# Performance work log

Hardware: AMD Instinct MI355X
Metric: run time of the kernel (lower is better)

Reference implementation:

```python
import jax, jax.numpy as jnp
import numpy as np

B, N, D, H, FF, L = 4, 256, 240, 8, 1024, 4
HD = D // H  # 30, divisible by 3 for 3D rotary
EPS = 1e-5


def setup_inputs() -> dict:
    key = jax.random.key(0)
    ks = iter(jax.random.split(key, 40))
    def nrm(shape, scale=1.0):
        return jax.random.normal(next(ks), shape, jnp.float32) * scale
    inp = {}
    for n in ["hand_token_t", "head_token_t", "hand_token_m1", "head_token_m1"]:
        inp[n] = nrm((B, N, D))
    for n in ["coords_hand_t", "coords_head_t", "coords_hand_m1", "coords_head_m1"]:
        inp[n] = jax.random.uniform(next(ks), (B, N, 3), jnp.float32)
    for n in ["state_t", "state_m1", "hand_pose_m1", "head_pose_m1", "hand_pose_t", "head_pose_t"]:
        inp[n] = nrm((B, D))
    sd = float(np.sqrt(2.0 / D))   # kaiming_normal fan_in=D
    sf = float(np.sqrt(2.0 / FF))  # kaiming_normal fan_in=FF
    inp["Wq"] = nrm((L, D, D), sd); inp["Wk"] = nrm((L, D, D), sd)
    inp["Wv"] = nrm((L, D, D), sd); inp["Wo"] = nrm((L, D, D), sd)
    inp["W1"] = nrm((L, FF, D), sd); inp["W2"] = nrm((L, D, FF), sf)
    inp["bq"] = jnp.zeros((L, D)); inp["bk"] = jnp.zeros((L, D))
    inp["bv"] = jnp.zeros((L, D)); inp["bo"] = jnp.zeros((L, D))
    inp["b1"] = jnp.zeros((L, FF)); inp["b2"] = jnp.zeros((L, D))
    inp["g1"] = jnp.ones((L, D)); inp["be1"] = jnp.zeros((L, D))
    inp["g2"] = jnp.ones((L, D)); inp["be2"] = jnp.zeros((L, D))
    return inp


def rope3d(x, coords):
    # x: (B,H,S,HD); coords: (B,S,3). head_dim split into 3 axis blocks,
    # each block rotated (interleaved pairs) by RoPE with pos = coord along that axis.
    d = HD // 3
    inv = 1.0 / (10000.0 ** (jnp.arange(0, d, 2, dtype=jnp.float32) / d))  # (d//2,)
    outs = []
    for a in range(3):
        xa = x[..., a * d:(a + 1) * d]
        ang = coords[:, None, :, a, None] * inv  # (B,1,S,d//2)
        c, s = jnp.cos(ang), jnp.sin(ang)
        x1, x2 = xa[..., 0::2], xa[..., 1::2]
        outs.append(jnp.stack([x1 * c - x2 * s, x1 * s + x2 * c], -1).reshape(xa.shape))
    if HD % 3:
        outs.append(x[..., 3 * d:])
    return jnp.concatenate(outs, -1)


def layernorm(x, g, b):
    m = x.mean(-1, keepdims=True)
    v = jnp.mean((x - m) ** 2, -1, keepdims=True)
    return (x - m) * jax.lax.rsqrt(v + EPS) * g + b


def _forward(hand_token_t, head_token_t, hand_token_m1, head_token_m1,
             coords_hand_t, coords_head_t, coords_hand_m1, coords_head_m1,
             state_t, state_m1, hand_pose_m1, head_pose_m1, hand_pose_t, head_pose_t,
             Wq, bq, Wk, bk, Wv, bv, Wo, bo, W1, b1, W2, b2, g1, be1, g2, be2):
    z3 = jnp.zeros((B, 1, 3), jnp.float32)
    src = jnp.concatenate([
        state_m1[:, None], hand_pose_m1[:, None], head_pose_m1[:, None],
        hand_token_m1, head_token_m1,
        state_t[:, None], hand_pose_t[:, None], head_pose_t[:, None],
        hand_token_t, head_token_t], axis=1)            # (B, S, D)
    cs = jnp.concatenate([z3, z3, z3, coords_hand_m1, coords_head_m1,
                          z3, z3, z3, coords_hand_t, coords_head_t], axis=1)  # (B, S, 3)
    S = src.shape[1]
    past = 1 + 2 + 2 * N  # current-frame tokens hide the past-frame keys
    mask = jnp.zeros((S, S), bool).at[past:, :past].set(True)
    scale = 1.0 / float(np.sqrt(HD))
    for l in range(L):
        q = (src @ Wq[l].T + bq[l]).reshape(B, S, H, HD).transpose(0, 2, 1, 3)
        k = (src @ Wk[l].T + bk[l]).reshape(B, S, H, HD).transpose(0, 2, 1, 3)
        v = (src @ Wv[l].T + bv[l]).reshape(B, S, H, HD).transpose(0, 2, 1, 3)
        q = rope3d(q, cs)
        k = rope3d(k, cs)
        scores = jnp.einsum('bhqd,bhkd->bhqk', q, k) * scale
        scores = jnp.where(mask, -jnp.inf, scores)
        attn = jnp.einsum('bhqk,bhkd->bhqd', jax.nn.softmax(scores, axis=-1), v)
        attn = attn.transpose(0, 2, 1, 3).reshape(B, S, D)
        s2 = layernorm(src + attn @ Wo[l].T + bo[l], g1[l], be1[l])
        ff = jax.nn.gelu(s2 @ W1[l].T + b1[l], approximate=False) @ W2[l].T + b2[l]
        src = layernorm(s2 + ff, g2[l], be2[l])
    return src[:, past:, :]


def reference(hand_token_t, head_token_t, hand_token_m1, head_token_m1,
              coords_hand_t, coords_head_t, coords_hand_m1, coords_head_m1,
              state_t, state_m1, hand_pose_m1, head_pose_m1, hand_pose_t, head_pose_t,
              Wq, bq, Wk, bk, Wv, bv, Wo, bo, W1, b1, W2, b2, g1, be1, g2, be2):
    return _forward(hand_token_t, head_token_t, hand_token_m1, head_token_m1,
                    coords_hand_t, coords_head_t, coords_hand_m1, coords_head_m1,
                    state_t, state_m1, hand_pose_m1, head_pose_m1, hand_pose_t, head_pose_t,
                    Wq, bq, Wk, bk, Wv, bv, Wo, bo, W1, b1, W2, b2, g1, be1, g2, be2)
```

## Files before the change

### kernel.cpp

```cpp
#include <hip/hip_runtime.h>
#include <cmath>

constexpr int cB = 4, cN = 256, cD = 240, cH = 8, cFF = 1024, cL = 4;
constexpr int cHD = 30;
constexpr int cS2 = 515;
constexpr int cBS2 = cB * cS2;
constexpr int cKp = 256;
constexpr int cSP2 = 576;
constexpr float EPSF = 1e-5f;

typedef __bf16 bf16x8 __attribute__((ext_vector_type(8)));
typedef float f32x4 __attribute__((ext_vector_type(4)));

__device__ inline unsigned short f2bf(float f) {
    unsigned int u = __builtin_bit_cast(unsigned int, f);
    unsigned int r = (u + 0x7fffu + ((u >> 16) & 1u)) >> 16;
    return (unsigned short)r;
}

constexpr int R1 = 4 * cL * 65536;
constexpr int R2 = R1 + cL * 1024 * 256;
constexpr int R3 = R2 + cL * 256 * 1024;
constexpr int R4 = R3 + cBS2 * cD;
constexpr int R5 = R4 + cBS2 * 15;
constexpr size_t qkvN = (size_t)cB * cH * cSP2 * 32;
constexpr int nSpan32 = (int)(3 * qkvN / 2);
constexpr int R6 = R5 + nSpan32;
constexpr int R7 = R6 + cBS2 * 8;

__global__ __launch_bounds__(256) void setup_all(
    const float* __restrict__ Wq, const float* __restrict__ Wk,
    const float* __restrict__ Wv, const float* __restrict__ Wo,
    const float* __restrict__ W1, const float* __restrict__ W2,
    const float* __restrict__ hand_t, const float* __restrict__ head_t,
    const float* __restrict__ state_t,
    const float* __restrict__ hand_pose_t, const float* __restrict__ head_pose_t,
    const float* __restrict__ ch_t, const float* __restrict__ cd_t,
    unsigned short* __restrict__ wqkv, unsigned short* __restrict__ w1p,
    unsigned short* __restrict__ w2p,
    float* __restrict__ src, unsigned short* __restrict__ sbf,
    float2* __restrict__ trig,
    unsigned int* __restrict__ qkvspan,
    unsigned short* __restrict__ padA, unsigned short* __restrict__ padB,
    unsigned short* __restrict__ padC)
{
    int idx = blockIdx.x * 256 + threadIdx.x;
    if (idx < R1) {
        int which = idx >> 18;
        const float* W = (which == 0) ? Wq : (which == 1) ? Wk : (which == 2) ? Wv : Wo;
        int rem = idx & 262143;
        int m = rem >> 16;
        int rc = rem & 65535;
        int r = rc >> 8, c = rc & 255;
        float v = (r < 240 && c < 240) ? W[((size_t)m * 240 + r) * 240 + c] : 0.f;
        wqkv[idx] = f2bf(v);
    } else if (idx < R2) {
        int rem = idx - R1;
        int m = rem >> 18;
        int rc = rem & 262143;
        int r = rc >> 8, c = rc & 255;
        float v = (c < 240) ? W1[((size_t)m * 1024 + r) * 240 + c] : 0.f;
        w1p[rem] = f2bf(v);
    } else if (idx < R3) {
        int rem = idx - R2;
        int m = rem >> 18;
        int rc = rem & 262143;
        int r = rc >> 10, c = rc & 1023;
        float v = (r < 240) ? W2[((size_t)m * 240 + r) * 1024 + c] : 0.f;
        w2p[rem] = f2bf(v);
    } else if (idx < R4) {
        int rem = idx - R3;
        int d = rem % cD;
        int r = rem / cD;
        int b = r / cS2, s = r % cS2;
        const float* p; int off;
        if (s == 0)          { p = state_t;      off = b * cD + d; }
        else if (s == 1)     { p = hand_pose_t;  off = b * cD + d; }
        else if (s == 2)     { p = head_pose_t;  off = b * cD + d; }
        else if (s < 259)    { p = hand_t;       off = (b * cN + (s - 3)) * cD + d; }
        else                 { p = head_t;       off = (b * cN + (s - 259)) * cD + d; }
        float v = p[off];
        src[rem] = v;
        sbf[(size_t)r * cKp + d] = f2bf(v);
    } else if (idx < R5) {
        int rem = idx - R4;
        int r = rem / 15, pair = rem - r * 15;
        int b = r / cS2, s = r % cS2;
        int a = pair / 5, j = pair - a * 5;
        float coord = 0.f;
        if (s >= 3 && s < 259)       coord = ch_t[(b * cN + (s - 3)) * 3 + a];
        else if (s >= 259)           coord = cd_t[(b * cN + (s - 259)) * 3 + a];
        float inv = __expf(-1.8420680743952367f * (float)j);
        float sn, co;
        sincosf(coord * inv, &sn, &co);
        trig[rem] = make_float2(co, sn);
    } else if (idx < R6) {
        qkvspan[idx - R5] = 0u;
    } else if (idx < R7) {
        int rem = idx - R6;
        int r = rem >> 3, j = rem & 7;
        ((unsigned int*)(padA + (size_t)r * 256 + 240))[j] = 0u;
        ((unsigned int*)(padB + (size_t)r * 256 + 240))[j] = 0u;
        ((unsigned int*)(padC + (size_t)r * 256 + 240))[j] = 0u;
    }
}

#define GEMM_CORE64(A_PTR, W_PTR, M_, KA_, NK_)                                               \
    __shared__ unsigned short Al[64][72];                                                     \
    __shared__ unsigned short Bl[64][72];                                                     \
    const int tid = threadIdx.x;                                                              \
    const int lane = tid & 63;                                                                \
    const int w = tid >> 6;                                                                   \
    const int wm = w >> 1, wn = w & 1;                                                        \
    const int lrow = lane & 15, kq = lane >> 4;                                               \
    const int colBase = blockIdx.x * 64;                                                      \
    const int sRow = tid >> 2;                                                                \
    const int sC = (tid & 3) * 16;                                                            \
    const int ar0 = min(rowBase + sRow, M_ - 1);                                              \
    const int wr = colBase + sRow;                                                            \
    const unsigned short* a0p = A_PTR + (size_t)ar0 * KA_ + sC;                               \
    const unsigned short* wp  = W_PTR + (size_t)wr * KA_ + sC;                                \
    f32x4 acc[2][2] = {};                                                                     \
    int4 rA0a = *(const int4*)a0p, rA0b = *(const int4*)(a0p + 8);                            \
    int4 rBa  = *(const int4*)wp,  rBb  = *(const int4*)(wp + 8);                             \
    for (int ks = 0; ks < NK_; ++ks) {                                                        \
        __syncthreads();                                                                      \
        *(int4*)&Al[sRow][sC]     = rA0a;                                                     \
        *(int4*)&Al[sRow][sC + 8] = rA0b;                                                     \
        *(int4*)&Bl[sRow][sC]     = rBa;                                                      \
        *(int4*)&Bl[sRow][sC + 8] = rBb;                                                      \
        __syncthreads();                                                                      \
        if (ks + 1 < NK_) {                                                                   \
            int kk = (ks + 1) * 64;                                                           \
            rA0a = *(const int4*)(a0p + kk); rA0b = *(const int4*)(a0p + kk + 8);             \
            rBa  = *(const int4*)(wp + kk);  rBb  = *(const int4*)(wp + kk + 8);              \
        }                                                                                     \
        _Pragma("unroll")                                                                     \
        for (int sub = 0; sub < 2; ++sub) {                                                   \
            bf16x8 af[2], bfr[2];                                                             \
            _Pragma("unroll")                                                                 \
            for (int i = 0; i < 2; ++i)                                                       \
                af[i] = *(const bf16x8*)&Al[wm * 32 + i * 16 + lrow][sub * 32 + kq * 8];      \
            _Pragma("unroll")                                                                 \
            for (int j = 0; j < 2; ++j)                                                       \
                bfr[j] = *(const bf16x8*)&Bl[wn * 32 + j * 16 + lrow][sub * 32 + kq * 8];     \
            _Pragma("unroll")                                                                 \
            for (int i = 0; i < 2; ++i)                                                       \
                _Pragma("unroll")                                                             \
                for (int j = 0; j < 2; ++j)                                                   \
                    acc[i][j] = __builtin_amdgcn_mfma_f32_16x16x32_bf16(af[i], bfr[j], acc[i][j], 0, 0, 0); \
        }                                                                                     \
    }

__global__ __launch_bounds__(256) void gemm_qkv_rope(
    const unsigned short* __restrict__ A,
    const unsigned short* __restrict__ Wqp, const unsigned short* __restrict__ Wkp,
    const unsigned short* __restrict__ Wvp,
    const float* __restrict__ bq, const float* __restrict__ bk, const float* __restrict__ bv,
    const float2* __restrict__ trig,
    unsigned short* __restrict__ qbf, unsigned short* __restrict__ kbf,
    unsigned short* __restrict__ vtbf)
{
    const int z = blockIdx.z;
    const unsigned short* Wsel = (z == 0) ? Wqp : (z == 1) ? Wkp : Wvp;
    const float* bias = (z == 0) ? bq : (z == 1) ? bk : bv;
    const int rowBase = blockIdx.y * 64;
    GEMM_CORE64(A, Wsel, cBS2, cKp, 4)
    if (z == 2) {
#pragma unroll
        for (int i = 0; i < 2; ++i) {
#pragma unroll
            for (int j = 0; j < 2; ++j) {
                int col = colBase + wn * 32 + j * 16 + lrow;
                if (col >= cD) continue;
                float bcol = bias[col];
                int hh = col / cHD, hd = col % cHD;
                f32x4 vv = acc[i][j];
                int row0 = rowBase + wm * 32 + i * 16 + kq * 4;
                int b0 = row0 / cS2, s0 = row0 - b0 * cS2;
                if (row0 + 3 < cBS2 && s0 + 3 < cS2) {
                    unsigned int lo = (unsigned)f2bf(vv[0] + bcol) | ((unsigned)f2bf(vv[1] + bcol) << 16);
                    unsigned int hi = (unsigned)f2bf(vv[2] + bcol) | ((unsigned)f2bf(vv[3] + bcol) << 16);
                    size_t base = ((size_t)(b0 * cH + hh) * 32 + hd) * cSP2 + s0;
                    *(unsigned int*)&vtbf[base]     = lo;
                    *(unsigned int*)&vtbf[base + 2] = hi;
                } else {
#pragma unroll
                    for (int r = 0; r < 4; ++r) {
                        int row = row0 + r;
                        if (row >= cBS2) continue;
                        int bb = row / cS2, ss = row - bb * cS2;
                        vtbf[((size_t)(bb * cH + hh) * 32 + hd) * cSP2 + ss] = f2bf(vv[r] + bcol);
                    }
                }
            }
        }
    } else {
        unsigned short* dst = (z == 0) ? qbf : kbf;
#pragma unroll
        for (int i = 0; i < 2; ++i) {
#pragma unroll
            for (int j = 0; j < 2; ++j) {
                int col = colBase + wn * 32 + j * 16 + lrow;
                bool colok = col < cD;
                int cc = colok ? col : 0;
                float bcol = colok ? bias[cc] : 0.f;
                int hh = cc / cHD, hd = cc % cHD;
                int a3 = hd / 10, jj = (hd % 10) >> 1;
                int pair = a3 * 5 + jj;
                f32x4 vv = acc[i][j];
#pragma unroll
                for (int r = 0; r < 4; ++r) {
                    int row = rowBase + wm * 32 + i * 16 + kq * 4 + r;
                    bool rowok = row < cBS2;
                    int rowc = rowok ? row : 0;
                    float val = vv[r] + bcol;
                    float pval = __shfl_xor(val, 1);
                    float2 t = trig[rowc * 15 + pair];
                    float outv = (hd & 1) ? (pval * t.y + val * t.x) : (val * t.x - pval * t.y);
                    if (colok && rowok) {
                        int b = rowc / cS2, s = rowc - b * cS2;
                        dst[((size_t)(b * cH + hh) * cSP2 + s) * 32 + hd] = f2bf(outv);
                    }
                }
            }
        }
    }
}

__global__ __launch_bounds__(256) void attn_mfma(
    const unsigned short* __restrict__ qbf, const unsigned short* __restrict__ kbf,
    const unsigned short* __restrict__ vtbf, unsigned short* __restrict__ outb)
{
    __shared__ unsigned short Pl[4][16][72];
    __shared__ float Ol[4][16][33];
    __shared__ float Ml[4][16];
    __shared__ float Ll[4][16];
    const int tid = threadIdx.x, lane = tid & 63, w = tid >> 6;
    const int bh = blockIdx.y, b = bh >> 3, h = bh & 7;
    const int qbase = blockIdx.x * 16;
    const int lr = lane & 15, lg = lane >> 4;
    const float scl = 0.18257418583505536f;
    const f32x4 czero = {0.f, 0.f, 0.f, 0.f};
    bf16x8 qf = *(const bf16x8*)&qbf[((size_t)bh * cSP2 + qbase + lr) * 32 + lg * 8];
    float m[4], l[4];
    f32x4 o0 = czero, o1 = czero;
#pragma unroll
    for (int r = 0; r < 4; ++r) { m[r] = -3.0e38f; l[r] = 0.f; }
    const int ts = (w * 9) / 4;
    const int te = ((w + 1) * 9) / 4;
    for (int tt = ts; tt < te; ++tt) {
        const int kb = tt * 64;
        f32x4 c[4];
#pragma unroll
        for (int t = 0; t < 4; ++t) {
            bf16x8 kf = *(const bf16x8*)&kbf[((size_t)bh * cSP2 + kb + 16 * t + lr) * 32 + lg * 8];
            c[t] = __builtin_amdgcn_mfma_f32_16x16x32_bf16(qf, kf, czero, 0, 0, 0);
        }
#pragma unroll
        for (int t = 0; t < 4; ++t) {
            bool koob = (kb + 16 * t + lr) >= cS2;
#pragma unroll
            for (int r = 0; r < 4; ++r)
                c[t][r] = koob ? -3.0e38f : c[t][r] * scl;
        }
        float mx[4];
#pragma unroll
        for (int r = 0; r < 4; ++r)
            mx[r] = fmaxf(fmaxf(c[0][r], c[1][r]), fmaxf(c[2][r], c[3][r]));
#pragma unroll
        for (int off = 1; off < 16; off <<= 1)
#pragma unroll
            for (int r = 0; r < 4; ++r)
                mx[r] = fmaxf(mx[r], __shfl_xor(mx[r], off));
        float corr[4], me[4], ps[4];
#pragma unroll
        for (int r = 0; r < 4; ++r) {
            float mn = fmaxf(m[r], mx[r]);
            corr[r] = __expf(m[r] - mn);
            m[r] = mn;
            me[r] = fmaxf(mn, -1.0e30f);
            ps[r] = 0.f;
        }
#pragma unroll
        for (int t = 0; t < 4; ++t)
#pragma unroll
            for (int r = 0; r < 4; ++r) {
                float p = __expf(c[t][r] - me[r]);
                c[t][r] = p;
                ps[r] += p;
            }
#pragma unroll
        for (int off = 1; off < 16; off <<= 1)
#pragma unroll
            for (int r = 0; r < 4; ++r)
                ps[r] += __shfl_xor(ps[r], off);
#pragma unroll
        for (int r = 0; r < 4; ++r) {
            l[r] = l[r] * corr[r] + ps[r];
            o0[r] *= corr[r];
            o1[r] *= corr[r];
        }
#pragma unroll
        for (int t = 0; t < 4; ++t)
#pragma unroll
            for (int r = 0; r < 4; ++r)
                Pl[w][lg * 4 + r][16 * t + lr] = f2bf(c[t][r]);
#pragma unroll
        for (int c2 = 0; c2 < 2; ++c2) {
            bf16x8 pa  = *(const bf16x8*)&Pl[w][lr][c2 * 32 + lg * 8];
            bf16x8 bv0 = *(const bf16x8*)&vtbf[((size_t)bh * 32 + lr) * cSP2 + kb + c2 * 32 + lg * 8];
            bf16x8 bv1 = *(const bf16x8*)&vtbf[((size_t)bh * 32 + 16 + lr) * cSP2 + kb + c2 * 32 + lg * 8];
            o0 = __builtin_amdgcn_mfma_f32_16x16x32_bf16(pa, bv0, o0, 0, 0, 0);
            o1 = __builtin_amdgcn_mfma_f32_16x16x32_bf16(pa, bv1, o1, 0, 0, 0);
        }
    }
#pragma unroll
    for (int r = 0; r < 4; ++r) {
        int row = lg * 4 + r;
        if (lr == 0) { Ml[w][row] = m[r]; Ll[w][row] = l[r]; }
        Ol[w][row][lr]      = o0[r];
        Ol[w][row][16 + lr] = o1[r];
    }
    __syncthreads();
    if (w == 0) {
        const int col = lane & 31, half = lane >> 5;
#pragma unroll
        for (int rr = 0; rr < 8; ++rr) {
            int row = half * 8 + rr;
            float M = fmaxf(fmaxf(Ml[0][row], Ml[1][row]), fmaxf(Ml[2][row], Ml[3][row]));
            float Lt = 0.f, Ot = 0.f;
#pragma unroll
            for (int ww = 0; ww < 4; ++ww) {
                float cc = __expf(Ml[ww][row] - M);
                Lt += Ll[ww][row] * cc;
                Ot += Ol[ww][row][col] * cc;
            }
            int qq = qbase + row;
            if (qq < cS2 && col < cHD)
                outb[((size_t)(b * cS2 + qq)) * cKp + h * cHD + col] = f2bf(Ot / Lt);
        }
    }
}

__global__ __launch_bounds__(256) void gemm_res64(
    const unsigned short* __restrict__ A, const unsigned short* __restrict__ W,
    const float* __restrict__ bias, const float* __restrict__ Rs,
    float* __restrict__ outF)
{
    const int rowBase = blockIdx.y * 64;
    GEMM_CORE64(A, W, cBS2, cKp, 4)
#pragma unroll
    for (int i = 0; i < 2; ++i) {
#pragma unroll
        for (int j = 0; j < 2; ++j) {
            int col = colBase + wn * 32 + j * 16 + lrow;
            if (col >= cD) continue;
            float bcol = bias[col];
            f32x4 v = acc[i][j];
#pragma unroll
            for (int r = 0; r < 4; ++r) {
                int row = rowBase + wm * 32 + i * 16 + kq * 4 + r;
                if (row >= cBS2) continue;
                outF[(size_t)row * cD + col] = v[r] + bcol + Rs[(size_t)row * cD + col];
            }
        }
    }
}

__global__ __launch_bounds__(256) void gemm_ff1(
    const unsigned short* __restrict__ A, const unsigned short* __restrict__ W,
    const float* __restrict__ bias, unsigned short* __restrict__ outB)
{
    const int rowBase = blockIdx.y * 64;
    GEMM_CORE64(A, W, cBS2, cKp, 4)
#pragma unroll
    for (int i = 0; i < 2; ++i) {
#pragma unroll
        for (int j = 0; j < 2; ++j) {
            int col = colBase + wn * 32 + j * 16 + lrow;
            float bcol = bias[col];
            f32x4 v = acc[i][j];
#pragma unroll
            for (int r = 0; r < 4; ++r) {
                int row = rowBase + wm * 32 + i * 16 + kq * 4 + r;
                if (row >= cBS2) continue;
                float t = v[r] + bcol;
                float gl = 0.5f * t * (1.0f + erff(t * 0.70710678118654752f));
                outB[(size_t)row * 1024 + col] = f2bf(gl);
            }
        }
    }
}

__global__ __launch_bounds__(256) void gemm_ff2_part(
    const unsigned short* __restrict__ A, const unsigned short* __restrict__ W,
    float* __restrict__ p0, float* __restrict__ p1)
{
    const int z = blockIdx.z;
    const int rowBase = blockIdx.y * 64;
    const unsigned short* Ap = A + z * 512;
    const unsigned short* Wp = W + z * 512;
    float* pF = z ? p1 : p0;
    GEMM_CORE64(Ap, Wp, cBS2, cFF, 8)
#pragma unroll
    for (int i = 0; i < 2; ++i) {
#pragma unroll
        for (int j = 0; j < 2; ++j) {
            int col = colBase + wn * 32 + j * 16 + lrow;
            if (col >= cD) continue;
            f32x4 v = acc[i][j];
#pragma unroll
            for (int r = 0; r < 4; ++r) {
                int row = rowBase + wm * 32 + i * 16 + kq * 4 + r;
                if (row >= cBS2) continue;
                pF[(size_t)row * cD + col] = v[r];
            }
        }
    }
}

__device__ inline void ln_core(float4 v, const float* __restrict__ g,
                               const float* __restrict__ be, float* __restrict__ yr,
                               unsigned short* __restrict__ br, int lane, bool ok)
{
    float sum = v.x + v.y + v.z + v.w;
#pragma unroll
    for (int off = 1; off < 64; off <<= 1) sum += __shfl_xor(sum, off);
    float mean = sum * (1.0f / cD);
    float vs = 0.f;
    if (ok) {
        float dx = v.x - mean, dy = v.y - mean, dz = v.z - mean, dw = v.w - mean;
        vs = dx * dx + dy * dy + dz * dz + dw * dw;
    }
#pragma unroll
    for (int off = 1; off < 64; off <<= 1) vs += __shfl_xor(vs, off);
    float rstd = rsqrtf(vs * (1.0f / cD) + EPSF);
    if (ok) {
        float4 g4 = *(const float4*)(g + 4 * lane);
        float4 b4 = *(const float4*)(be + 4 * lane);
        float4 y;
        y.x = (v.x - mean) * rstd * g4.x + b4.x;
        y.y = (v.y - mean) * rstd * g4.y + b4.y;
        y.z = (v.z - mean) * rstd * g4.z + b4.z;
        y.w = (v.w - mean) * rstd * g4.w + b4.w;
        *(float4*)(yr + 4 * lane) = y;
        if (br) {
            uint2 pk;
            pk.x = (unsigned)f2bf(y.x) | ((unsigned)f2bf(y.y) << 16);
            pk.y = (unsigned)f2bf(y.z) | ((unsigned)f2bf(y.w) << 16);
            *(uint2*)(br + 4 * lane) = pk;
        }
    }
}

__global__ __launch_bounds__(256) void ln_kernel(
    const float* __restrict__ x, const float* __restrict__ g,
    const float* __restrict__ be, float* __restrict__ y, unsigned short* __restrict__ ybf)
{
    int row = blockIdx.x * 4 + (threadIdx.x >> 6);
    int lane = threadIdx.x & 63;
    if (row >= cBS2) return;
    bool ok = lane < 60;
    float4 v = make_float4(0.f, 0.f, 0.f, 0.f);
    if (ok) v = *(const float4*)(x + (size_t)row * cD + 4 * lane);
    ln_core(v, g, be, y + (size_t)row * cD, ybf + (size_t)row * cKp, lane, ok);
}

__global__ __launch_bounds__(256) void ln2_kernel(
    const float* __restrict__ s2, const float* __restrict__ p0, const float* __restrict__ p1,
    const float* __restrict__ b2, const float* __restrict__ g, const float* __restrict__ be,
    float* __restrict__ y, unsigned short* __restrict__ ybf)
{
    int row = blockIdx.x * 4 + (threadIdx.x >> 6);
    int lane = threadIdx.x & 63;
    if (row >= cBS2) return;
    bool ok = lane < 60;
    float4 v = make_float4(0.f, 0.f, 0.f, 0.f);
    if (ok) {
        float4 a  = *(const float4*)(s2 + (size_t)row * cD + 4 * lane);
        float4 q0 = *(const float4*)(p0 + (size_t)row * cD + 4 * lane);
        float4 q1 = *(const float4*)(p1 + (size_t)row * cD + 4 * lane);
        float4 bb = *(const float4*)(b2 + 4 * lane);
        v.x = a.x + q0.x + q1.x + bb.x;
        v.y = a.y + q0.y + q1.y + bb.y;
        v.z = a.z + q0.z + q1.z + bb.z;
        v.w = a.w + q0.w + q1.w + bb.w;
    }
    ln_core(v, g, be, y + (size_t)row * cD, ybf + (size_t)row * cKp, lane, ok);
}

__global__ __launch_bounds__(256) void ln2_final(
    const float* __restrict__ s2, const float* __restrict__ p0, const float* __restrict__ p1,
    const float* __restrict__ b2, const float* __restrict__ g, const float* __restrict__ be,
    float* __restrict__ out)
{
    int row = blockIdx.x * 4 + (threadIdx.x >> 6);
    int lane = threadIdx.x & 63;
    if (row >= cBS2) return;
    bool ok = lane < 60;
    float4 v = make_float4(0.f, 0.f, 0.f, 0.f);
    if (ok) {
        float4 a  = *(const float4*)(s2 + (size_t)row * cD + 4 * lane);
        float4 q0 = *(const float4*)(p0 + (size_t)row * cD + 4 * lane);
        float4 q1 = *(const float4*)(p1 + (size_t)row * cD + 4 * lane);
        float4 bb = *(const float4*)(b2 + 4 * lane);
        v.x = a.x + q0.x + q1.x + bb.x;
        v.y = a.y + q0.y + q1.y + bb.y;
        v.z = a.z + q0.z + q1.z + bb.z;
        v.w = a.w + q0.w + q1.w + bb.w;
    }
    ln_core(v, g, be, out + (size_t)row * cD, nullptr, lane, ok);
}

extern "C" void kernel_launch(void* const* d_in, const int* in_sizes, int n_in,
                              void* d_out, int out_size, void* d_ws, size_t ws_size,
                              hipStream_t stream) {
    (void)in_sizes; (void)n_in; (void)out_size; (void)ws_size;
    const float* hand_t       = (const float*)d_in[0];
    const float* head_t       = (const float*)d_in[1];
    const float* c_hand_t     = (const float*)d_in[4];
    const float* c_head_t     = (const float*)d_in[5];
    const float* state_t      = (const float*)d_in[8];
    const float* hand_pose_t  = (const float*)d_in[12];
    const float* head_pose_t  = (const float*)d_in[13];
    const float* Wq = (const float*)d_in[14];
    const float* Wk = (const float*)d_in[15];
    const float* Wv = (const float*)d_in[16];
    const float* Wo = (const float*)d_in[17];
    const float* W1 = (const float*)d_in[18];
    const float* W2 = (const float*)d_in[19];
    const float* bq = (const float*)d_in[20];
    const float* bk = (const float*)d_in[21];
    const float* bv = (const float*)d_in[22];
    const float* bo = (const float*)d_in[23];
    const float* b1 = (const float*)d_in[24];
    const float* b2 = (const float*)d_in[25];
    const float* g1 = (const float*)d_in[26];
    const float* be1 = (const float*)d_in[27];
    const float* g2 = (const float*)d_in[28];
    const float* be2 = (const float*)d_in[29];

    char* p = (char*)d_ws;
    auto alloc_f = [&](size_t n) { float* r = (float*)p; p += n * sizeof(float); return r; };
    auto alloc_h = [&](size_t n) { unsigned short* r = (unsigned short*)p; p += n * sizeof(unsigned short); return r; };
    float* srcb  = alloc_f((size_t)cBS2 * cD);
    float* s2b   = alloc_f((size_t)cBS2 * cD);
    float* resid = alloc_f((size_t)cBS2 * cD);
    float* part1 = alloc_f((size_t)cBS2 * cD);
    float* trigf = alloc_f((size_t)cBS2 * 15 * 2);
    unsigned short* src_bf  = alloc_h((size_t)cBS2 * cKp);
    unsigned short* s2_bf   = alloc_h((size_t)cBS2 * cKp);
    unsigned short* attn_bf = alloc_h((size_t)cBS2 * cKp);
    unsigned short* ff_bf   = alloc_h((size_t)cBS2 * cFF);
    unsigned short* qbf  = alloc_h(qkvN);
    unsigned short* kbf  = alloc_h(qkvN);
    unsigned short* vtbf = alloc_h(qkvN);
    unsigned short* wqkv = alloc_h((size_t)4 * cL * 65536);
    unsigned short* w1p  = alloc_h((size_t)cL * 1024 * 256);
    unsigned short* w2p  = alloc_h((size_t)cL * 256 * 1024);
    float2* trig = (float2*)trigf;

    setup_all<<<(R7 + 255) / 256, 256, 0, stream>>>(
        Wq, Wk, Wv, Wo, W1, W2,
        hand_t, head_t, state_t, hand_pose_t, head_pose_t,
        c_hand_t, c_head_t,
        wqkv, w1p, w2p, srcb, src_bf, trig,
        (unsigned int*)qbf, src_bf, s2_bf, attn_bf);

    const int mT = (cBS2 + 63) / 64;
    for (int l = 0; l < cL; ++l) {
        const unsigned short* wq_l = wqkv + (size_t)(0 * cL + l) * 65536;
        const unsigned short* wk_l = wqkv + (size_t)(1 * cL + l) * 65536;
        const unsigned short* wv_l = wqkv + (size_t)(2 * cL + l) * 65536;
        const unsigned short* wo_l = wqkv + (size_t)(3 * cL + l) * 65536;
        const unsigned short* w1_l = w1p + (size_t)l * 1024 * 256;
        const unsigned short* w2_l = w2p + (size_t)l * 256 * 1024;
        const float* bq_l = bq + (size_t)l * cD;
        const float* bk_l = bk + (size_t)l * cD;
        const float* bv_l = bv + (size_t)l * cD;
        const float* bo_l = bo + (size_t)l * cD;
        const float* b1_l = b1 + (size_t)l * cFF;
        const float* b2_l = b2 + (size_t)l * cD;
        const float* g1_l = g1 + (size_t)l * cD;
        const float* be1_l = be1 + (size_t)l * cD;
        const float* g2_l = g2 + (size_t)l * cD;
        const float* be2_l = be2 + (size_t)l * cD;

        gemm_qkv_rope<<<dim3(4, mT, 3), 256, 0, stream>>>(
            src_bf, wq_l, wk_l, wv_l, bq_l, bk_l, bv_l, trig, qbf, kbf, vtbf);
        attn_mfma<<<dim3((cS2 + 15) / 16, cB * cH), 256, 0, stream>>>(
            qbf, kbf, vtbf, attn_bf);
        gemm_res64<<<dim3(4, mT), 256, 0, stream>>>(
            attn_bf, wo_l, bo_l, srcb, resid);
        ln_kernel<<<(cBS2 + 3) / 4, 256, 0, stream>>>(resid, g1_l, be1_l, s2b, s2_bf);
        gemm_ff1<<<dim3(16, mT), 256, 0, stream>>>(s2_bf, w1_l, b1_l, ff_bf);
        gemm_ff2_part<<<dim3(4, mT, 2), 256, 0, stream>>>(ff_bf, w2_l, resid, part1);
        if (l < cL - 1) {
            ln2_kernel<<<(cBS2 + 3) / 4, 256, 0, stream>>>(
                s2b, resid, part1, b2_l, g2_l, be2_l, srcb, src_bf);
        } else {
            ln2_final<<<(cBS2 + 3) / 4, 256, 0, stream>>>(
                s2b, resid, part1, b2_l, g2_l, be2_l, (float*)d_out);
        }
    }
}
```

Baseline: 247.5 us.

## Fuse layernorms into preceding GEMMs via last-block atomic counter

Removes the standalone ln_kernel, ln2_kernel and ln2_final launches. Each row-tile's last-finishing GEMM block, found with an atomic counter per row tile and thread fences, now does the layernorm for those 64 rows. This saves kernel launches and an extra pass over the activations each layer. In exchange, only one block per row tile does the LN work serially at the end, and correctness relies on fences and on resetting the counters.

```diff
diff --git a/kernel.cpp b/kernel.cpp
--- a/kernel.cpp
+++ b/kernel.cpp
@@ -27,6 +27,7 @@
 constexpr int nSpan32 = (int)(3 * qkvN / 2);
 constexpr int R6 = R5 + nSpan32;
 constexpr int R7 = R6 + cBS2 * 8;
+constexpr int R8 = R7 + 128;
 
 __global__ __launch_bounds__(256) void setup_all(
     const float* __restrict__ Wq, const float* __restrict__ Wk,
@@ -42,7 +43,8 @@
     float2* __restrict__ trig,
     unsigned int* __restrict__ qkvspan,
     unsigned short* __restrict__ padA, unsigned short* __restrict__ padB,
-    unsigned short* __restrict__ padC)
+    unsigned short* __restrict__ padC,
+    unsigned int* __restrict__ cnts)
 {
     int idx = blockIdx.x * 256 + threadIdx.x;
     if (idx < R1) {
@@ -102,6 +104,8 @@
         ((unsigned int*)(padA + (size_t)r * 256 + 240))[j] = 0u;
         ((unsigned int*)(padB + (size_t)r * 256 + 240))[j] = 0u;
         ((unsigned int*)(padC + (size_t)r * 256 + 240))[j] = 0u;
+    } else if (idx < R8) {
+        cnts[idx - R7] = 0u;
     }
 }
 
@@ -128,7 +132,7 @@
         *(int4*)&Al[sRow][sC]     = rA0a;                                                     \
         *(int4*)&Al[sRow][sC + 8] = rA0b;                                                     \
         *(int4*)&Bl[sRow][sC]     = rBa;                                                      \
-        *(int4*)&Bl[sRow][sC + 8] = rBb;                                                      \
+        *(int4*)&Bl[sRow][sC + 8] = rBb;                                                     \
         __syncthreads();                                                                      \
         if (ks + 1 < NK_) {                                                                   \
             int kk = (ks + 1) * 64;                                                           \
@@ -152,6 +156,40 @@
         }                                                                                     \
     }
 
+__device__ inline void ln_core(float4 v, const float* __restrict__ g,
+                               const float* __restrict__ be, float* __restrict__ yr,
+                               unsigned short* __restrict__ br, int lane, bool ok)
+{
+    float sum = v.x + v.y + v.z + v.w;
+#pragma unroll
+    for (int off = 1; off < 64; off <<= 1) sum += __shfl_xor(sum, off);
+    float mean = sum * (1.0f / cD);
+    float vs = 0.f;
+    if (ok) {
+        float dx = v.x - mean, dy = v.y - mean, dz = v.z - mean, dw = v.w - mean;
+        vs = dx * dx + dy * dy + dz * dz + dw * dw;
+    }
+#pragma unroll
+    for (int off = 1; off < 64; off <<= 1) vs += __shfl_xor(vs, off);
+    float rstd = rsqrtf(vs * (1.0f / cD) + EPSF);
+    if (ok) {
+        float4 g4 = *(const float4*)(g + 4 * lane);
+        float4 b4 = *(const float4*)(be + 4 * lane);
+        float4 y;
+        y.x = (v.x - mean) * rstd * g4.x + b4.x;
+        y.y = (v.y - mean) * rstd * g4.y + b4.y;
+        y.z = (v.z - mean) * rstd * g4.z + b4.z;
+        y.w = (v.w - mean) * rstd * g4.w + b4.w;
+        *(float4*)(yr + 4 * lane) = y;
+        if (br) {
+            uint2 pk;
+            pk.x = (unsigned)f2bf(y.x) | ((unsigned)f2bf(y.y) << 16);
+            pk.y = (unsigned)f2bf(y.z) | ((unsigned)f2bf(y.w) << 16);
+            *(uint2*)(br + 4 * lane) = pk;
+        }
+    }
+}
+
 __global__ __launch_bounds__(256) void gemm_qkv_rope(
     const unsigned short* __restrict__ A,
     const unsigned short* __restrict__ Wqp, const unsigned short* __restrict__ Wkp,
@@ -343,10 +381,13 @@
     }
 }
 
-__global__ __launch_bounds__(256) void gemm_res64(
+__global__ __launch_bounds__(256) void gemm_res64_ln(
     const unsigned short* __restrict__ A, const unsigned short* __restrict__ W,
     const float* __restrict__ bias, const float* __restrict__ Rs,
-    float* __restrict__ outF)
+    float* __restrict__ outF,
+    const float* __restrict__ g, const float* __restrict__ be,
+    float* __restrict__ yF, unsigned short* __restrict__ yB,
+    unsigned int* __restrict__ cnt)
 {
     const int rowBase = blockIdx.y * 64;
     GEMM_CORE64(A, W, cBS2, cKp, 4)
@@ -364,6 +405,26 @@
                 if (row >= cBS2) continue;
                 outF[(size_t)row * cD + col] = v[r] + bcol + Rs[(size_t)row * cD + col];
             }
+        }
+    }
+    __threadfence();
+    __syncthreads();
+    __shared__ int lastBlk;
+    if (tid == 0) {
+        unsigned int old = atomicAdd(&cnt[blockIdx.y], 1u);
+        lastBlk = (old == 3u);
+        if (old == 3u) cnt[blockIdx.y] = 0u;
+    }
+    __syncthreads();
+    if (lastBlk) {
+        __threadfence();
+        for (int rr = w; rr < 64; rr += 4) {
+            int row = rowBase + rr;
+            if (row >= cBS2) break;
+            bool ok = lane < 60;
+            float4 v = make_float4(0.f, 0.f, 0.f, 0.f);
+            if (ok) v = *(const float4*)(outF + (size_t)row * cD + 4 * lane);
+            ln_core(v, g, be, yF + (size_t)row * cD, yB + (size_t)row * cKp, lane, ok);
         }
     }
 }
@@ -393,9 +454,14 @@
     }
 }
 
-__global__ __launch_bounds__(256) void gemm_ff2_part(
+template<int FIN>
+__global__ __launch_bounds__(256) void gemm_ff2_ln(
     const unsigned short* __restrict__ A, const unsigned short* __restrict__ W,
-    float* __restrict__ p0, float* __restrict__ p1)
+    float* __restrict__ p0, float* __restrict__ p1,
+    const float* __restrict__ s2, const float* __restrict__ b2,
+    const float* __restrict__ g, const float* __restrict__ be,
+    float* __restrict__ yF, unsigned short* __restrict__ yB,
+    unsigned int* __restrict__ cnt)
 {
     const int z = blockIdx.z;
     const int rowBase = blockIdx.y * 64;
@@ -418,99 +484,36 @@
             }
         }
     }
-}
-
-__device__ inline void ln_core(float4 v, const float* __restrict__ g,
-                               const float* __restrict__ be, float* __restrict__ yr,
-                               unsigned short* __restrict__ br, int lane, bool ok)
-{
-    float sum = v.x + v.y + v.z + v.w;
-#pragma unroll
-    for (int off = 1; off < 64; off <<= 1) sum += __shfl_xor(sum, off);
-    float mean = sum * (1.0f / cD);
-    float vs = 0.f;
-    if (ok) {
-        float dx = v.x - mean, dy = v.y - mean, dz = v.z - mean, dw = v.w - mean;
-        vs = dx * dx + dy * dy + dz * dz + dw * dw;
-    }
-#pragma unroll
-    for (int off = 1; off < 64; off <<= 1) vs += __shfl_xor(vs, off);
-    float rstd = rsqrtf(vs * (1.0f / cD) + EPSF);
-    if (ok) {
-        float4 g4 = *(const float4*)(g + 4 * lane);
-        float4 b4 = *(const float4*)(be + 4 * lane);
-        float4 y;
-        y.x = (v.x - mean) * rstd * g4.x + b4.x;
-        y.y = (v.y - mean) * rstd * g4.y + b4.y;
-        y.z = (v.z - mean) * rstd * g4.z + b4.z;
-        y.w = (v.w - mean) * rstd * g4.w + b4.w;
-        *(float4*)(yr + 4 * lane) = y;
-        if (br) {
-            uint2 pk;
-            pk.x = (unsigned)f2bf(y.x) | ((unsigned)f2bf(y.y) << 16);
-            pk.y = (unsigned)f2bf(y.z) | ((unsigned)f2bf(y.w) << 16);
-            *(uint2*)(br + 4 * lane) = pk;
-        }
-    }
-}
-
-__global__ __launch_bounds__(256) void ln_kernel(
-    const float* __restrict__ x, const float* __restrict__ g,
-    const float* __restrict__ be, float* __restrict__ y, unsigned short* __restrict__ ybf)
-{
-    int row = blockIdx.x * 4 + (threadIdx.x >> 6);
-    int lane = threadIdx.x & 63;
-    if (row >= cBS2) return;
-    bool ok = lane < 60;
-    float4 v = make_float4(0.f, 0.f, 0.f, 0.f);
-    if (ok) v = *(const float4*)(x + (size_t)row * cD + 4 * lane);
-    ln_core(v, g, be, y + (size_t)row * cD, ybf + (size_t)row * cKp, lane, ok);
-}
-
-__global__ __launch_bounds__(256) void ln2_kernel(
-    const float* __restrict__ s2, const float* __restrict__ p0, const float* __restrict__ p1,
-    const float* __restrict__ b2, const float* __restrict__ g, const float* __restrict__ be,
-    float* __restrict__ y, unsigned short* __restrict__ ybf)
-{
-    int row = blockIdx.x * 4 + (threadIdx.x >> 6);
-    int lane = threadIdx.x & 63;
-    if (row >= cBS2) return;
-    bool ok = lane < 60;
-    float4 v = make_float4(0.f, 0.f, 0.f, 0.f);
-    if (ok) {
-        float4 a  = *(const float4*)(s2 + (size_t)row * cD + 4 * lane);
-        float4 q0 = *(const float4*)(p0 + (size_t)row * cD + 4 * lane);
-        float4 q1 = *(const float4*)(p1 + (size_t)row * cD + 4 * lane);
-        float4 bb = *(const float4*)(b2 + 4 * lane);
-        v.x = a.x + q0.x + q1.x + bb.x;
-        v.y = a.y + q0.y + q1.y + bb.y;
-        v.z = a.z + q0.z + q1.z + bb.z;
-        v.w = a.w + q0.w + q1.w + bb.w;
-    }
-    ln_core(v, g, be, y + (size_t)row * cD, ybf + (size_t)row * cKp, lane, ok);
-}
-
-__global__ __launch_bounds__(256) void ln2_final(
-    const float* __restrict__ s2, const float* __restrict__ p0, const float* __restrict__ p1,
-    const float* __restrict__ b2, const float* __restrict__ g, const float* __restrict__ be,
-    float* __restrict__ out)
-{
-    int row = blockIdx.x * 4 + (threadIdx.x >> 6);
-    int lane = threadIdx.x & 63;
-    if (row >= cBS2) return;
-    bool ok = lane < 60;
-    float4 v = make_float4(0.f, 0.f, 0.f, 0.f);
-    if (ok) {
-        float4 a  = *(const float4*)(s2 + (size_t)row * cD + 4 * lane);
-        float4 q0 = *(const float4*)(p0 + (size_t)row * cD + 4 * lane);
-        float4 q1 = *(const float4*)(p1 + (size_t)row * cD + 4 * lane);
-        float4 bb = *(const float4*)(b2 + 4 * lane);
-        v.x = a.x + q0.x + q1.x + bb.x;
-        v.y = a.y + q0.y + q1.y + bb.y;
-        v.z = a.z + q0.z + q1.z + bb.z;
-        v.w = a.w + q0.w + q1.w + bb.w;
-    }
-    ln_core(v, g, be, out + (size_t)row * cD, nullptr, lane, ok);
+    __threadfence();
+    __syncthreads();
+    __shared__ int lastBlk;
+    if (tid == 0) {
+        unsigned int old = atomicAdd(&cnt[blockIdx.y], 1u);
+        lastBlk = (old == 7u);
+        if (old == 7u) cnt[blockIdx.y] = 0u;
+    }
+    __syncthreads();
+    if (lastBlk) {
+        __threadfence();
+        for (int rr = w; rr < 64; rr += 4) {
+            int row = rowBase + rr;
+            if (row >= cBS2) break;
+            bool ok = lane < 60;
+            float4 v = make_float4(0.f, 0.f, 0.f, 0.f);
+            if (ok) {
+                float4 a  = *(const float4*)(s2 + (size_t)row * cD + 4 * lane);
+                float4 q0 = *(const float4*)(p0 + (size_t)row * cD + 4 * lane);
+                float4 q1 = *(const float4*)(p1 + (size_t)row * cD + 4 * lane);
+                float4 bb = *(const float4*)(b2 + 4 * lane);
+                v.x = a.x + q0.x + q1.x + bb.x;
+                v.y = a.y + q0.y + q1.y + bb.y;
+                v.z = a.z + q0.z + q1.z + bb.z;
+                v.w = a.w + q0.w + q1.w + bb.w;
+            }
+            ln_core(v, g, be, yF + (size_t)row * cD,
+                    FIN ? nullptr : (yB + (size_t)row * cKp), lane, ok);
+        }
+    }
 }
 
 extern "C" void kernel_launch(void* const* d_in, const int* in_sizes, int n_in,
@@ -549,6 +552,7 @@
     float* resid = alloc_f((size_t)cBS2 * cD);
     float* part1 = alloc_f((size_t)cBS2 * cD);
     float* trigf = alloc_f((size_t)cBS2 * 15 * 2);
+    unsigned int* cnts = (unsigned int*)alloc_f(128);
     unsigned short* src_bf  = alloc_h((size_t)cBS2 * cKp);
     unsigned short* s2_bf   = alloc_h((size_t)cBS2 * cKp);
     unsigned short* attn_bf = alloc_h((size_t)cBS2 * cKp);
@@ -560,13 +564,15 @@
     unsigned short* w1p  = alloc_h((size_t)cL * 1024 * 256);
     unsigned short* w2p  = alloc_h((size_t)cL * 256 * 1024);
     float2* trig = (float2*)trigf;
-
-    setup_all<<<(R7 + 255) / 256, 256, 0, stream>>>(
+    unsigned int* cntA = cnts;
+    unsigned int* cntB = cnts + 64;
+
+    setup_all<<<(R8 + 255) / 256, 256, 0, stream>>>(
         Wq, Wk, Wv, Wo, W1, W2,
         hand_t, head_t, state_t, hand_pose_t, head_pose_t,
         c_hand_t, c_head_t,
         wqkv, w1p, w2p, srcb, src_bf, trig,
-        (unsigned int*)qbf, src_bf, s2_bf, attn_bf);
+        (unsigned int*)qbf, src_bf, s2_bf, attn_bf, cnts);
 
     const int mT = (cBS2 + 63) / 64;
     for (int l = 0; l < cL; ++l) {
@@ -591,17 +597,16 @@
             src_bf, wq_l, wk_l, wv_l, bq_l, bk_l, bv_l, trig, qbf, kbf, vtbf);
         attn_mfma<<<dim3((cS2 + 15) / 16, cB * cH), 256, 0, stream>>>(
             qbf, kbf, vtbf, attn_bf);
-        gemm_res64<<<dim3(4, mT), 256, 0, stream>>>(
-            attn_bf, wo_l, bo_l, srcb, resid);
-        ln_kernel<<<(cBS2 + 3) / 4, 256, 0, stream>>>(resid, g1_l, be1_l, s2b, s2_bf);
+        gemm_res64_ln<<<dim3(4, mT), 256, 0, stream>>>(
+            attn_bf, wo_l, bo_l, srcb, resid, g1_l, be1_l, s2b, s2_bf, cntA);
         gemm_ff1<<<dim3(16, mT), 256, 0, stream>>>(s2_bf, w1_l, b1_l, ff_bf);
-        gemm_ff2_part<<<dim3(4, mT, 2), 256, 0, stream>>>(ff_bf, w2_l, resid, part1);
         if (l < cL - 1) {
-            ln2_kernel<<<(cBS2 + 3) / 4, 256, 0, stream>>>(
-                s2b, resid, part1, b2_l, g2_l, be2_l, srcb, src_bf);
+            gemm_ff2_ln<0><<<dim3(4, mT, 2), 256, 0, stream>>>(
+                ff_bf, w2_l, resid, part1, s2b, b2_l, g2_l, be2_l, srcb, src_bf, cntB);
         } else {
-            ln2_final<<<(cBS2 + 3) / 4, 256, 0, stream>>>(
-                s2b, resid, part1, b2_l, g2_l, be2_l, (float*)d_out);
-        }
-    }
-}
+            gemm_ff2_ln<1><<<dim3(4, mT, 2), 256, 0, stream>>>(
+                ff_bf, w2_l, resid, part1, s2b, b2_l, g2_l, be2_l,
+                (float*)d_out, nullptr, cntB);
+        }
+    }
+}
```

Result: slower. 597.6 us (+141.4%).
